# Optimization experiments

Measured on AMD Instinct MI355X. Metric: run time of the kernel, lower is better.

The kernel has to match this reference:

```python
import jax, jax.numpy as jnp
import numpy as np

N, M, T_STEPS = 32, 64, 20000  # t = T/dt = 200/0.01
DT = 0.01
SQRT_DT = DT ** 0.5


def setup_inputs() -> dict:
    key = jax.random.key(0)
    k1, k2 = jax.random.split(key)
    # theta ~ U(lower, upper) per the module's prior (4-param variant)
    lower = jnp.array([0.5, 0.1, 0.1, 0.0], dtype=jnp.float32)
    upper = jnp.array([1.5, 3.0, 0.6, 4.0], dtype=jnp.float32)
    theta = lower + (upper - lower) * jax.random.uniform(k1, (N, 4), dtype=jnp.float32)
    noise = jax.random.normal(k2, (N, M, T_STEPS), dtype=jnp.float32)
    return {"theta": theta, "noise": noise}


def reference(theta, noise):
    # Euler-Maruyama OU recurrence: x_{i+1} = x_i + gamma*(mu - x_i)*dt + sigma*sqrt(dt)*eps_i
    n, m, t = noise.shape
    gamma = theta[:, 0][:, None]  # [n,1] broadcasts over m
    mu = theta[:, 1][:, None]
    sigma = theta[:, 2][:, None]
    x0 = jnp.broadcast_to(theta[:, 3][:, None], (n, m))

    eps_t = jnp.moveaxis(noise, -1, 0)  # [t, n, m] for scan

    def step(x, eps):
        x_new = x + gamma * (mu - x) * DT + sigma * SQRT_DT * eps
        return x_new, x_new

    _, xs = jax.lax.scan(step, x0, eps_t)  # xs: [t, n, m] == x[:, :, 1:]
    return jnp.moveaxis(xs, 0, -1)  # [n, m, t]
```

## Files before the change

### kernel.cpp

```cpp
#include <hip/hip_runtime.h>


#define T_STEPS 20000
#define M_PATHS 64
#define CHUNK   4
#define NWAVES  8
#define BLOCK   (NWAVES * 64)
#define BTILE   (BLOCK * CHUNK)
#define NBT     ((T_STEPS + BTILE - 1) / BTILE)
#define DT      0.01f
#define SQRT_DT 0.1f

typedef float f32x4 __attribute__((ext_vector_type(4)));

__global__ __launch_bounds__(BLOCK, 8) void ou_scan_kernel(
    const float* __restrict__ theta,
    const float* __restrict__ noise,
    float* __restrict__ out)
{
    __shared__ float sB[2][NWAVES];

    const int tid   = threadIdx.x;
    const int wave  = tid >> 6;
    const int lane  = tid & 63;
    const int chain = blockIdx.x;
    const int n     = chain >> 6;

    const float gamma = theta[n * 4 + 0];
    const float mu    = theta[n * 4 + 1];
    const float sigma = theta[n * 4 + 2];
    float carry       = theta[n * 4 + 3];

    const float a    = 1.0f - gamma * DT;
    const float gmdt = gamma * mu * DT;
    const float ssd  = sigma * SQRT_DT;

    const float a2    = a * a;
    const float a4    = a2 * a2;
    const float a8    = a4 * a4;
    const float a16   = a8 * a8;
    const float a32   = a16 * a16;
    const float a64   = a32 * a32;
    const float a128  = a64 * a64;
    const float a256  = a128 * a128;
    const float a512  = a256 * a256;
    const float a1024 = a512 * a512;
    const float a2048 = a1024 * a1024;

    float Aex = 1.f;
    if (lane & 1)  Aex *= a4;
    if (lane & 2)  Aex *= a8;
    if (lane & 4)  Aex *= a16;
    if (lane & 8)  Aex *= a32;
    if (lane & 16) Aex *= a64;
    if (lane & 32) Aex *= a128;

    float PA = 1.f;
    if (wave & 1) PA *= a256;
    if (wave & 2) PA *= a512;
    if (wave & 4) PA *= a1024;
    const float FA = a2048;

    const float* __restrict__ np_ = noise + (size_t)chain * T_STEPS;
    float* __restrict__       op_ = out   + (size_t)chain * T_STEPS;

    float4 c = *(const float4*)(np_ + tid * CHUNK);

    for (int tb = 0; tb < NBT; ++tb) {
        float4 nx = make_float4(0.f, 0.f, 0.f, 0.f);
        const int ne0 = (tb + 1) * BTILE + tid * CHUNK;
        if (ne0 + CHUNK <= T_STEPS) nx = *(const float4*)(np_ + ne0);

        const int  base = tb * BTILE + tid * CHUNK;
        const bool act  = (base + CHUNK <= T_STEPS);

        const float b0 = fmaf(ssd, c.x, gmdt);
        const float b1 = fmaf(ssd, c.y, gmdt);
        const float b2 = fmaf(ssd, c.z, gmdt);
        const float b3 = fmaf(ssd, c.w, gmdt);

        float p = b0;
        p = fmaf(p, a, b1);
        p = fmaf(p, a, b2);
        p = fmaf(p, a, b3);

        float B = act ? p : 0.f;

        {
            float t;
            t = __shfl_up(B, 1);  if (lane >= 1)  B = fmaf(a4,   t, B);
            t = __shfl_up(B, 2);  if (lane >= 2)  B = fmaf(a8,   t, B);
            t = __shfl_up(B, 4);  if (lane >= 4)  B = fmaf(a16,  t, B);
            t = __shfl_up(B, 8);  if (lane >= 8)  B = fmaf(a32,  t, B);
            t = __shfl_up(B, 16); if (lane >= 16) B = fmaf(a64,  t, B);
            t = __shfl_up(B, 32); if (lane >= 32) B = fmaf(a128, t, B);
        }

        if (lane == 63) sB[tb & 1][wave] = B;
        __syncthreads();

        float PB = 0.f, pb = 0.f;
        #pragma unroll
        for (int v = 0; v < NWAVES; ++v) {
            if (v == wave) PB = pb;
            pb = fmaf(pb, a256, sB[tb & 1][v]);
        }

        const float xw = fmaf(PA, carry, PB);

        float Bex = __shfl_up(B, 1);
        if (lane == 0) Bex = 0.f;
        float x = fmaf(Aex, xw, Bex);

        carry = fmaf(FA, carry, pb);

        if (act) {
            f32x4 o;
            x = fmaf(a, x, b0); o.x = x;
            x = fmaf(a, x, b1); o.y = x;
            x = fmaf(a, x, b2); o.z = x;
            x = fmaf(a, x, b3); o.w = x;
            __builtin_nontemporal_store(o, (f32x4*)(op_ + base));
        }

        c = nx;
    }
}

extern "C" void kernel_launch(void* const* d_in, const int* in_sizes, int n_in,
                              void* d_out, int out_size, void* d_ws, size_t ws_size,
                              hipStream_t stream) {
    const float* theta = (const float*)d_in[0];
    const float* noise = (const float*)d_in[1];
    float* out = (float*)d_out;

    const int chains = in_sizes[1] / T_STEPS;
    ou_scan_kernel<<<chains, BLOCK, 0, stream>>>(theta, noise, out);
}
```

Measured before the change: 287.5 us.

## Give each wave a contiguous segment with register-resident noise and one block barrier

Restructures the scan so each wave owns a contiguous 2560-step segment. Its noise stays in registers for ten rounds, and a first pass reduces the segment to a single affine sum that one barrier combines across waves. The per-tile __syncthreads and shared-memory carry chain of the old block-wide loop go away, and each wave carries its own state across rounds with a shuffle. In exchange it holds 40 noise floats per thread, lowers the launch-bounds occupancy hint, and recomputes the per-chunk partials twice.

```diff
diff --git a/kernel.cpp b/kernel.cpp
--- a/kernel.cpp
+++ b/kernel.cpp
@@ -3,22 +3,21 @@
 
 #define T_STEPS 20000
 #define M_PATHS 64
-#define CHUNK   4
 #define NWAVES  8
 #define BLOCK   (NWAVES * 64)
-#define BTILE   (BLOCK * CHUNK)
-#define NBT     ((T_STEPS + BTILE - 1) / BTILE)
+#define SEG     2560
+#define ROUNDS  10
 #define DT      0.01f
 #define SQRT_DT 0.1f
 
 typedef float f32x4 __attribute__((ext_vector_type(4)));
 
-__global__ __launch_bounds__(BLOCK, 8) void ou_scan_kernel(
+__global__ __launch_bounds__(BLOCK, 4) void ou_scan_kernel(
     const float* __restrict__ theta,
     const float* __restrict__ noise,
     float* __restrict__ out)
 {
-    __shared__ float sB[2][NWAVES];
+    __shared__ float sS[NWAVES];
 
     const int tid   = threadIdx.x;
     const int wave  = tid >> 6;
@@ -29,7 +28,7 @@
     const float gamma = theta[n * 4 + 0];
     const float mu    = theta[n * 4 + 1];
     const float sigma = theta[n * 4 + 2];
-    float carry       = theta[n * 4 + 3];
+    const float x0    = theta[n * 4 + 3];
 
     const float a    = 1.0f - gamma * DT;
     const float gmdt = gamma * mu * DT;
@@ -46,6 +45,16 @@
     const float a512  = a256 * a256;
     const float a1024 = a512 * a512;
     const float a2048 = a1024 * a1024;
+    const float a2560 = a2048 * a512;
+
+    const int li = lane ^ 63;
+    float wred = 1.f;
+    if (li & 1)  wred *= a4;
+    if (li & 2)  wred *= a8;
+    if (li & 4)  wred *= a16;
+    if (li & 8)  wred *= a32;
+    if (li & 16) wred *= a64;
+    if (li & 32) wred *= a128;
 
     float Aex = 1.f;
     if (lane & 1)  Aex *= a4;
@@ -55,36 +64,77 @@
     if (lane & 16) Aex *= a64;
     if (lane & 32) Aex *= a128;
 
-    float PA = 1.f;
-    if (wave & 1) PA *= a256;
-    if (wave & 2) PA *= a512;
-    if (wave & 4) PA *= a1024;
-    const float FA = a2048;
-
     const float* __restrict__ np_ = noise + (size_t)chain * T_STEPS;
     float* __restrict__       op_ = out   + (size_t)chain * T_STEPS;
+    const int segb = wave * SEG;
+    const int loff = lane << 2;
 
-    float4 c = *(const float4*)(np_ + tid * CHUNK);
+    float4 c[ROUNDS];
+    #pragma unroll
+    for (int r = 0; r < ROUNDS; ++r) {
+        const int e = segb + (r << 8) + loff;
+        if (e + 4 <= T_STEPS) {
+            c[r] = *(const float4*)(np_ + e);
+        } else {
+            c[r] = make_float4(0.f, 0.f, 0.f, 0.f);
+        }
+    }
 
-    for (int tb = 0; tb < NBT; ++tb) {
-        float4 nx = make_float4(0.f, 0.f, 0.f, 0.f);
-        const int ne0 = (tb + 1) * BTILE + tid * CHUNK;
-        if (ne0 + CHUNK <= T_STEPS) nx = *(const float4*)(np_ + ne0);
+    float acc = 0.f;
+    #pragma unroll
+    for (int r = 0; r < ROUNDS; ++r) {
+        const int  e  = segb + (r << 8) + loff;
+        const bool ar = (e + 4 <= T_STEPS);
+        const float b0 = fmaf(ssd, c[r].x, gmdt);
+        const float b1 = fmaf(ssd, c[r].y, gmdt);
+        const float b2 = fmaf(ssd, c[r].z, gmdt);
+        const float b3 = fmaf(ssd, c[r].w, gmdt);
+        float p = b0;
+        p = fmaf(p, a, b1);
+        p = fmaf(p, a, b2);
+        p = fmaf(p, a, b3);
+        acc = fmaf(acc, a256, ar ? p : 0.f);
+    }
+    {
+        float v = wred * acc;
+        v += __shfl_xor(v, 1);
+        v += __shfl_xor(v, 2);
+        v += __shfl_xor(v, 4);
+        v += __shfl_xor(v, 8);
+        v += __shfl_xor(v, 16);
+        v += __shfl_xor(v, 32);
+        if (lane == 0) sS[wave] = v;
+    }
 
-        const int  base = tb * BTILE + tid * CHUNK;
-        const bool act  = (base + CHUNK <= T_STEPS);
+    __syncthreads();
 
-        const float b0 = fmaf(ssd, c.x, gmdt);
-        const float b1 = fmaf(ssd, c.y, gmdt);
-        const float b2 = fmaf(ssd, c.z, gmdt);
-        const float b3 = fmaf(ssd, c.w, gmdt);
+    float xw;
+    {
+        float xs = x0;
+        float my = x0;
+        #pragma unroll
+        for (int v = 0; v < NWAVES; ++v) {
+            if (wave == v) my = xs;
+            xs = fmaf(a2560, xs, sS[v]);
+        }
+        xw = my;
+    }
 
+    #pragma unroll
+    for (int r = 0; r < ROUNDS; ++r) {
+        const int  e  = segb + (r << 8) + loff;
+        const bool ar = (e + 4 <= T_STEPS);
+
+        const float b0 = fmaf(ssd, c[r].x, gmdt);
+        const float b1 = fmaf(ssd, c[r].y, gmdt);
+        const float b2 = fmaf(ssd, c[r].z, gmdt);
+        const float b3 = fmaf(ssd, c[r].w, gmdt);
         float p = b0;
         p = fmaf(p, a, b1);
         p = fmaf(p, a, b2);
         p = fmaf(p, a, b3);
 
-        float B = act ? p : 0.f;
+        float B = ar ? p : 0.f;
 
         {
             float t;
@@ -96,34 +146,21 @@
             t = __shfl_up(B, 32); if (lane >= 32) B = fmaf(a128, t, B);
         }
 
-        if (lane == 63) sB[tb & 1][wave] = B;
-        __syncthreads();
-
-        float PB = 0.f, pb = 0.f;
-        #pragma unroll
-        for (int v = 0; v < NWAVES; ++v) {
-            if (v == wave) PB = pb;
-            pb = fmaf(pb, a256, sB[tb & 1][v]);
-        }
-
-        const float xw = fmaf(PA, carry, PB);
-
         float Bex = __shfl_up(B, 1);
         if (lane == 0) Bex = 0.f;
         float x = fmaf(Aex, xw, Bex);
 
-        carry = fmaf(FA, carry, pb);
+        const float B63 = __shfl(B, 63);
+        xw = fmaf(a256, xw, B63);
 
-        if (act) {
+        if (ar) {
             f32x4 o;
             x = fmaf(a, x, b0); o.x = x;
             x = fmaf(a, x, b1); o.y = x;
             x = fmaf(a, x, b2); o.z = x;
             x = fmaf(a, x, b3); o.w = x;
-            __builtin_nontemporal_store(o, (f32x4*)(op_ + base));
+            __builtin_nontemporal_store(o, (f32x4*)(op_ + e));
         }
-
-        c = nx;
     }
 }
 
```

New measurement: 285.2 us. No clear change (-0.8%).

## Assign one wave per chain and prefetch noise with double-buffered register tiles

Applied to the files above, without the earlier changes.

Each wave now processes a whole chain sequentially in 256-element tiles, carrying state with a wave-level shuffle. This replaces the block-wide scan, which needed shared memory and a __syncthreads every tile. Noise is loaded in groups of 16 tiles into two register buffers so loads overlap compute. The cost is a much longer serial dependency chain per wave, fewer blocks, and high register pressure from 32 float4 buffers.

```diff
diff --git a/kernel.cpp b/kernel.cpp
--- a/kernel.cpp
+++ b/kernel.cpp
@@ -3,49 +3,44 @@
 
 #define T_STEPS 20000
 #define M_PATHS 64
-#define CHUNK   4
-#define NWAVES  8
+#define NWAVES  4
 #define BLOCK   (NWAVES * 64)
-#define BTILE   (BLOCK * CHUNK)
-#define NBT     ((T_STEPS + BTILE - 1) / BTILE)
+#define TILE_F  256
+#define NTILES  80
+#define DEPTH   16
 #define DT      0.01f
 #define SQRT_DT 0.1f
 
 typedef float f32x4 __attribute__((ext_vector_type(4)));
 
-__global__ __launch_bounds__(BLOCK, 8) void ou_scan_kernel(
+__global__ __launch_bounds__(BLOCK, 2) void ou_scan_kernel(
     const float* __restrict__ theta,
     const float* __restrict__ noise,
     float* __restrict__ out)
 {
-    __shared__ float sB[2][NWAVES];
-
     const int tid   = threadIdx.x;
     const int wave  = tid >> 6;
     const int lane  = tid & 63;
-    const int chain = blockIdx.x;
+    const int chain = blockIdx.x * NWAVES + wave;
     const int n     = chain >> 6;
 
     const float gamma = theta[n * 4 + 0];
     const float mu    = theta[n * 4 + 1];
     const float sigma = theta[n * 4 + 2];
-    float carry       = theta[n * 4 + 3];
+    float xw          = theta[n * 4 + 3];
 
     const float a    = 1.0f - gamma * DT;
     const float gmdt = gamma * mu * DT;
     const float ssd  = sigma * SQRT_DT;
 
-    const float a2    = a * a;
-    const float a4    = a2 * a2;
-    const float a8    = a4 * a4;
-    const float a16   = a8 * a8;
-    const float a32   = a16 * a16;
-    const float a64   = a32 * a32;
-    const float a128  = a64 * a64;
-    const float a256  = a128 * a128;
-    const float a512  = a256 * a256;
-    const float a1024 = a512 * a512;
-    const float a2048 = a1024 * a1024;
+    const float a2   = a * a;
+    const float a4   = a2 * a2;
+    const float a8   = a4 * a4;
+    const float a16  = a8 * a8;
+    const float a32  = a16 * a16;
+    const float a64  = a32 * a32;
+    const float a128 = a64 * a64;
+    const float a256 = a128 * a128;
 
     float Aex = 1.f;
     if (lane & 1)  Aex *= a4;
@@ -55,37 +50,30 @@
     if (lane & 16) Aex *= a64;
     if (lane & 32) Aex *= a128;
 
-    float PA = 1.f;
-    if (wave & 1) PA *= a256;
-    if (wave & 2) PA *= a512;
-    if (wave & 4) PA *= a1024;
-    const float FA = a2048;
-
     const float* __restrict__ np_ = noise + (size_t)chain * T_STEPS;
     float* __restrict__       op_ = out   + (size_t)chain * T_STEPS;
+    const int loff = lane << 2;
 
-    float4 c = *(const float4*)(np_ + tid * CHUNK);
+    auto ld = [&](const int tile) -> float4 {
+        const int e = tile * TILE_F + loff;
+        if (e + 4 <= T_STEPS) return *(const float4*)(np_ + e);
+        return make_float4(0.f, 0.f, 0.f, 0.f);
+    };
 
-    for (int tb = 0; tb < NBT; ++tb) {
-        float4 nx = make_float4(0.f, 0.f, 0.f, 0.f);
-        const int ne0 = (tb + 1) * BTILE + tid * CHUNK;
-        if (ne0 + CHUNK <= T_STEPS) nx = *(const float4*)(np_ + ne0);
+    auto do_tile = [&](const float4 cv, const int tile) {
+        const int  e   = tile * TILE_F + loff;
+        const bool act = (e + 4 <= T_STEPS);
 
-        const int  base = tb * BTILE + tid * CHUNK;
-        const bool act  = (base + CHUNK <= T_STEPS);
-
-        const float b0 = fmaf(ssd, c.x, gmdt);
-        const float b1 = fmaf(ssd, c.y, gmdt);
-        const float b2 = fmaf(ssd, c.z, gmdt);
-        const float b3 = fmaf(ssd, c.w, gmdt);
-
+        const float b0 = fmaf(ssd, cv.x, gmdt);
+        const float b1 = fmaf(ssd, cv.y, gmdt);
+        const float b2 = fmaf(ssd, cv.z, gmdt);
+        const float b3 = fmaf(ssd, cv.w, gmdt);
         float p = b0;
         p = fmaf(p, a, b1);
         p = fmaf(p, a, b2);
         p = fmaf(p, a, b3);
 
         float B = act ? p : 0.f;
-
         {
             float t;
             t = __shfl_up(B, 1);  if (lane >= 1)  B = fmaf(a4,   t, B);
@@ -96,23 +84,12 @@
             t = __shfl_up(B, 32); if (lane >= 32) B = fmaf(a128, t, B);
         }
 
-        if (lane == 63) sB[tb & 1][wave] = B;
-        __syncthreads();
-
-        float PB = 0.f, pb = 0.f;
-        #pragma unroll
-        for (int v = 0; v < NWAVES; ++v) {
-            if (v == wave) PB = pb;
-            pb = fmaf(pb, a256, sB[tb & 1][v]);
-        }
-
-        const float xw = fmaf(PA, carry, PB);
-
         float Bex = __shfl_up(B, 1);
         if (lane == 0) Bex = 0.f;
         float x = fmaf(Aex, xw, Bex);
 
-        carry = fmaf(FA, carry, pb);
+        const float B63 = __shfl(B, 63);
+        xw = fmaf(a256, xw, B63);
 
         if (act) {
             f32x4 o;
@@ -120,10 +97,40 @@
             x = fmaf(a, x, b1); o.y = x;
             x = fmaf(a, x, b2); o.z = x;
             x = fmaf(a, x, b3); o.w = x;
-            __builtin_nontemporal_store(o, (f32x4*)(op_ + base));
+            __builtin_nontemporal_store(o, (f32x4*)(op_ + e));
         }
+    };
 
-        c = nx;
+    float4 cA[DEPTH], cB[DEPTH];
+    #pragma unroll
+    for (int s = 0; s < DEPTH; ++s) {
+        cA[s] = make_float4(0.f, 0.f, 0.f, 0.f);
+        cB[s] = make_float4(0.f, 0.f, 0.f, 0.f);
+    }
+
+    #pragma unroll
+    for (int s = 0; s < DEPTH; ++s) cA[s] = ld(s);
+    __builtin_amdgcn_sched_barrier(0);
+
+    #pragma unroll
+    for (int g = 0; g < 5; ++g) {
+        if (g < 4) {
+            if (g & 1) {
+                #pragma unroll
+                for (int s = 0; s < DEPTH; ++s) cA[s] = ld((g + 1) * DEPTH + s);
+            } else {
+                #pragma unroll
+                for (int s = 0; s < DEPTH; ++s) cB[s] = ld((g + 1) * DEPTH + s);
+            }
+        }
+        __builtin_amdgcn_sched_barrier(0);
+        if (g & 1) {
+            #pragma unroll
+            for (int s = 0; s < DEPTH; ++s) do_tile(cB[s], g * DEPTH + s);
+        } else {
+            #pragma unroll
+            for (int s = 0; s < DEPTH; ++s) do_tile(cA[s], g * DEPTH + s);
+        }
     }
 }
 
@@ -135,5 +142,6 @@
     float* out = (float*)d_out;
 
     const int chains = in_sizes[1] / T_STEPS;
-    ou_scan_kernel<<<chains, BLOCK, 0, stream>>>(theta, noise, out);
+    const int blocks = chains / NWAVES;
+    ou_scan_kernel<<<blocks, BLOCK, 0, stream>>>(theta, noise, out);
 }
```

Result: no change. 292.0 us (+1.5%).
